# Kernel optimization log

Hardware: AMD Instinct MI355X
Metric: run time of the kernel (lower is better)

The kernel has to match this reference:

```python
import jax, jax.numpy as jnp
import numpy as np

B, N, M, P, LQK, LV, DQK, DV = 2, 512, 50, 2, 9, 9, 32, 32
K = DQK // 2  # theta frequencies; repeat_interleave(theta,2) must match last dim of q/k


def setup_inputs() -> dict:
    key = jax.random.key(0)
    ks = jax.random.split(key, 7)
    q = jax.random.normal(ks[0], (B, N, P, LQK, DQK), dtype=jnp.float32)
    k = jax.random.normal(ks[1], (B, N, P, LQK, DQK), dtype=jnp.float32)
    v = jax.random.normal(ks[2], (B, N, P, LV, DV), dtype=jnp.float32)
    pos = jax.random.normal(ks[3], (B, N, 3), dtype=jnp.float32) * 3.0  # atom coords
    u = jax.random.normal(ks[4], (B, M, 3), dtype=jnp.float32)
    grid_u = u / jnp.linalg.norm(u, axis=-1, keepdims=True)  # unit-sphere Lebedev points
    grid_w = jax.random.uniform(ks[5], (B, M), dtype=jnp.float32) / M  # quadrature weights
    theta = jax.random.uniform(ks[6], (K,), dtype=jnp.float32)
    return {"q": q, "k": k, "v": v, "pos": pos, "grid_u": grid_u, "grid_w": grid_w, "theta": theta}


def apply_erope(x, pos, grid_u, theta):
    # x: [B,N,P,L,H]; pos: [B,N,3]; grid_u: [B,M,3]; theta: [K], H = 2K
    proj = jnp.einsum('bnd,bmd->bmn', pos, grid_u)           # [B,M,N]
    rep_theta = jnp.repeat(theta, 2)                          # [H]
    ang = proj[..., None] * rep_theta                         # [B,M,N,H]
    sin, cos = jnp.sin(ang), jnp.cos(ang)
    # rotate pairs: (x0,x1) -> (-x1, x0) interleaved
    xs = jnp.stack([-x[..., 1::2], x[..., ::2]], axis=-1).reshape(x.shape)
    return (jnp.einsum('bNPLH,bMNH->bMNPLH', x, cos)
            + jnp.einsum('bNPLH,bMNH->bMNPLH', xs, sin))      # [B,M,N,P,L,H]


def reference(q, k, v, pos, grid_u, grid_w, theta):
    qr = apply_erope(q, pos, grid_u, theta)  # [B,M,N,P,L,Dqk]
    kr = apply_erope(k, pos, grid_u, theta)
    b, m, n = qr.shape[:3]
    qf = qr.reshape(b, m, n, -1)             # [B,M,N,t], t = P*L*Dqk
    kf = kr.reshape(b, m, n, -1)
    vf = v.reshape(v.shape[0], v.shape[1], -1)  # [B,N,qdim]
    qf = qf / (qf.shape[-1] ** 0.5)
    # Exactly equals torch's kv=einsum('bMNt,bNq->bMNtq'); y=einsum('bMNt,bMNtq,bM->bMNq')
    # without materializing the [B,M,N,t,q] outer product.
    y = jnp.einsum('bMNt,bMNt,bNq,bM->bMNq', qf, kf, vf, grid_w)
    return y.reshape(b, m, n, *v.shape[2:])   # [B,M,N,P,LV,DV]
```

## Files before the change

kernel.cpp:

```cpp
#include <hip/hip_runtime.h>

#define BQ     2
#define NN     512
#define MM     50
#define TDIM   576
#define T4     144
#define SPLIT  2
#define MSPLIT (MM / SPLIT)

typedef float f4 __attribute__((ext_vector_type(4)));

__global__ void __launch_bounds__(256) erope_fused_kernel(
        const float* __restrict__ q,
        const float* __restrict__ k,
        const float* __restrict__ v,
        const float* __restrict__ w,
        float* __restrict__ out) {
    const int blk   = blockIdx.x;
    const int split = blk & (SPLIT - 1);
    const int row   = blk >> 1;
    const int b     = row >> 9;
    const int n     = row & (NN - 1);
    const int t     = threadIdx.x;

    __shared__ f4    vsh[T4];
    __shared__ float red[4];
    __shared__ float dsh;

    float acc = 0.0f;
    if (t < T4) {
        const f4 a = ((const f4*)(q + (size_t)row * TDIM))[t];
        const f4 c = ((const f4*)(k + (size_t)row * TDIM))[t];
        vsh[t] = ((const f4*)(v + (size_t)row * TDIM))[t];
        acc = a.x * c.x + a.y * c.y + a.z * c.z + a.w * c.w;
    }
    #pragma unroll
    for (int off = 32; off > 0; off >>= 1)
        acc += __shfl_down(acc, off, 64);
    if ((t & 63) == 0) red[t >> 6] = acc;
    __syncthreads();
    if (t == 0) dsh = (red[0] + red[1] + red[2] + red[3]) * (1.0f / 24.0f);
    __syncthreads();
    const float dval = dsh;

    const float* wrow = w + b * MM + split * MSPLIT;
    f4* const outbase = (f4*)out
        + ((size_t)(b * MM + split * MSPLIT) * NN + n) * T4;
    const size_t mstride = (size_t)NN * T4;

    for (int i = t; i < MSPLIT * T4; i += 256) {
        const int ml = i / T4;
        const int qi = i - ml * T4;
        const float s = dval * wrow[ml];
        const f4 vv = vsh[qi];
        outbase[(size_t)ml * mstride + qi] = vv * s;
    }
}

extern "C" void kernel_launch(void* const* d_in, const int* in_sizes, int n_in,
                              void* d_out, int out_size, void* d_ws, size_t ws_size,
                              hipStream_t stream) {
    const float* q   = (const float*)d_in[0];
    const float* k   = (const float*)d_in[1];
    const float* v   = (const float*)d_in[2];
    const float* w   = (const float*)d_in[5];
    float*       out = (float*)d_out;

    erope_fused_kernel<<<BQ * NN * SPLIT, 256, 0, stream>>>(q, k, v, w, out);
}
```

Before: 25.90 us.

## Map each row-split unit to one wavefront with a persistent grid

Each row/split unit of work is now handled by a single 64-lane wavefront instead of a 256-thread block. The q·k dot product is reduced with wave shuffles only, with no shared memory or block barriers, and the v row stays in registers. A fixed grid of 1024 waves loops over the 2048 units, and the per-m store loop is fully unrolled. The aim is to cut barrier and LDS overhead and the integer division in the store loop. The cost is fewer waves in flight to drive a store stream that is bandwidth-bound, plus idle lanes in the 16-lane tail.

```diff
diff --git a/kernel.cpp b/kernel.cpp
--- a/kernel.cpp
+++ b/kernel.cpp
@@ -7,53 +7,59 @@
 #define T4     144
 #define SPLIT  2
 #define MSPLIT (MM / SPLIT)
+#define UNITS  (BQ * NN * SPLIT)
+#define NWAVES 1024
 
 typedef float f4 __attribute__((ext_vector_type(4)));
 
-__global__ void __launch_bounds__(256) erope_fused_kernel(
+__global__ void __launch_bounds__(256) erope_wave_kernel(
         const float* __restrict__ q,
         const float* __restrict__ k,
         const float* __restrict__ v,
         const float* __restrict__ w,
         float* __restrict__ out) {
-    const int blk   = blockIdx.x;
-    const int split = blk & (SPLIT - 1);
-    const int row   = blk >> 1;
-    const int b     = row >> 9;
-    const int n     = row & (NN - 1);
-    const int t     = threadIdx.x;
+    const int gwave = blockIdx.x * 4 + (threadIdx.x >> 6);
+    const int lane  = threadIdx.x & 63;
 
-    __shared__ f4    vsh[T4];
-    __shared__ float red[4];
-    __shared__ float dsh;
+    for (int u = gwave; u < UNITS; u += NWAVES) {
+        const int split = u & (SPLIT - 1);
+        const int row   = u >> 1;
+        const int b     = row >> 9;
+        const int n     = row & (NN - 1);
 
-    float acc = 0.0f;
-    if (t < T4) {
-        const f4 a = ((const f4*)(q + (size_t)row * TDIM))[t];
-        const f4 c = ((const f4*)(k + (size_t)row * TDIM))[t];
-        vsh[t] = ((const f4*)(v + (size_t)row * TDIM))[t];
-        acc = a.x * c.x + a.y * c.y + a.z * c.z + a.w * c.w;
-    }
-    #pragma unroll
-    for (int off = 32; off > 0; off >>= 1)
-        acc += __shfl_down(acc, off, 64);
-    if ((t & 63) == 0) red[t >> 6] = acc;
-    __syncthreads();
-    if (t == 0) dsh = (red[0] + red[1] + red[2] + red[3]) * (1.0f / 24.0f);
-    __syncthreads();
-    const float dval = dsh;
+        const f4* q4 = (const f4*)(q + (size_t)row * TDIM);
+        const f4* k4 = (const f4*)(k + (size_t)row * TDIM);
+        const f4* v4 = (const f4*)(v + (size_t)row * TDIM);
 
-    const float* wrow = w + b * MM + split * MSPLIT;
-    f4* const outbase = (f4*)out
-        + ((size_t)(b * MM + split * MSPLIT) * NN + n) * T4;
-    const size_t mstride = (size_t)NN * T4;
+        f4 a0 = q4[lane],      c0 = k4[lane];
+        f4 a1 = q4[lane + 64], c1 = k4[lane + 64];
+        f4 v0 = v4[lane],      v1 = v4[lane + 64];
+        f4 v2 = {0.f, 0.f, 0.f, 0.f};
+        float acc = a0.x*c0.x + a0.y*c0.y + a0.z*c0.z + a0.w*c0.w
+                  + a1.x*c1.x + a1.y*c1.y + a1.z*c1.z + a1.w*c1.w;
+        if (lane < 16) {
+            f4 a2 = q4[lane + 128], c2 = k4[lane + 128];
+            v2 = v4[lane + 128];
+            acc += a2.x*c2.x + a2.y*c2.y + a2.z*c2.z + a2.w*c2.w;
+        }
+        #pragma unroll
+        for (int off = 32; off > 0; off >>= 1)
+            acc += __shfl_xor(acc, off, 64);
+        const float dval = acc * (1.0f / 24.0f);
 
-    for (int i = t; i < MSPLIT * T4; i += 256) {
-        const int ml = i / T4;
-        const int qi = i - ml * T4;
-        const float s = dval * wrow[ml];
-        const f4 vv = vsh[qi];
-        outbase[(size_t)ml * mstride + qi] = vv * s;
+        const float* wp = w + b * MM + split * MSPLIT;
+        f4* ob = (f4*)out
+               + ((size_t)(b * MM + split * MSPLIT) * NN + n) * T4 + lane;
+        const size_t mstride = (size_t)NN * T4;
+
+        #pragma unroll
+        for (int ml = 0; ml < MSPLIT; ++ml) {
+            const float s = dval * wp[ml];
+            f4* p = ob + (size_t)ml * mstride;
+            p[0]   = v0 * s;
+            p[64]  = v1 * s;
+            if (lane < 16) p[128] = v2 * s;
+        }
     }
 }
 
@@ -66,5 +72,5 @@
     const float* w   = (const float*)d_in[5];
     float*       out = (float*)d_out;
 
-    erope_fused_kernel<<<BQ * NN * SPLIT, 256, 0, stream>>>(q, k, v, w, out);
+    erope_wave_kernel<<<NWAVES / 4, 256, 0, stream>>>(q, k, v, w, out);
 }
```

New measurement: 25.37 us. 2.1% less time.
